# Kernel tuning notes

Hardware: AMD Instinct MI355X
Metric: run time of the kernel (lower is better)

## Reference

```python
import jax, jax.numpy as jnp
import numpy as np

DIM = 256
H = W = 56
WS = 7           # window size
SHIFT = 3        # shift size
NH = 8           # num heads
HD = DIM // NH   # head dim
N = WS * WS      # tokens per window
SCALE = HD ** -0.5
EPS = 1e-5


def _rel_pos_index():
    coords = np.stack(np.meshgrid(np.arange(WS), np.arange(WS), indexing='ij'))  # (2,WS,WS)
    cf = coords.reshape(2, -1)                                # (2, N)
    rel = cf[:, :, None] - cf[:, None, :]                     # (2, N, N)
    rel = rel.transpose(1, 2, 0).astype(np.int64)             # (N, N, 2)
    rel[:, :, 0] += WS - 1
    rel[:, :, 1] += WS - 1
    rel[:, :, 0] *= 2 * WS - 1
    return rel.sum(-1)                                        # (N, N)

REL_IDX = _rel_pos_index()


def _attn_mask():
    # standard Swin shift mask: (nW, N, N) with 0 / -100
    img = np.zeros((H, W))
    cnt = 0
    for hs in (slice(0, -WS), slice(-WS, -SHIFT), slice(-SHIFT, None)):
        for ws in (slice(0, -WS), slice(-WS, -SHIFT), slice(-SHIFT, None)):
            img[hs, ws] = cnt
            cnt += 1
    win = img.reshape(H // WS, WS, W // WS, WS).transpose(0, 2, 1, 3).reshape(-1, N)  # (nW, N)
    diff = win[:, None, :] - win[:, :, None]
    return np.where(diff != 0, -100.0, 0.0).astype(np.float32)

ATTN_MASK = jnp.asarray(_attn_mask())  # (nW, N, N)


def _ln(x, g, b):
    mu = jnp.mean(x, -1, keepdims=True)
    var = jnp.mean(jnp.square(x - mu), -1, keepdims=True)
    return (x - mu) * jax.lax.rsqrt(var + EPS) * g + b


def _win_part(x):
    # (B,H,W,C) -> (B*nW, N, C)
    B, _, _, C = x.shape
    x = x.reshape(B, H // WS, WS, W // WS, WS, C)
    return x.transpose(0, 1, 3, 2, 4, 5).reshape(-1, N, C)


def _win_rev(xw, B):
    # (B*nW, N, C) -> (B,H,W,C)
    C = xw.shape[-1]
    x = xw.reshape(B, H // WS, W // WS, WS, WS, C)
    return x.transpose(0, 1, 3, 2, 4, 5).reshape(B, H, W, C)


def setup_inputs() -> dict:
    key = jax.random.key(0)
    ks = jax.random.split(key, 6)
    return {
        'x': jax.random.normal(ks[0], (32, H * W, DIM), jnp.float32),
        'norm1_g': jnp.ones((DIM,), jnp.float32),
        'norm1_b': jnp.zeros((DIM,), jnp.float32),
        'qkv_w': jax.random.normal(ks[1], (3 * DIM, DIM), jnp.float32) * 0.02,
        'qkv_b': jnp.zeros((3 * DIM,), jnp.float32),
        'rel_table': jax.random.normal(ks[2], ((2 * WS - 1) ** 2, NH), jnp.float32) * 0.02,
        'proj_w': jax.random.normal(ks[3], (DIM, DIM), jnp.float32) * 0.02,
        'proj_b': jnp.zeros((DIM,), jnp.float32),
        'norm2_g': jnp.ones((DIM,), jnp.float32),
        'norm2_b': jnp.zeros((DIM,), jnp.float32),
        'fc1_w': jax.random.normal(ks[4], (4 * DIM, DIM), jnp.float32) * 0.02,
        'fc1_b': jnp.zeros((4 * DIM,), jnp.float32),
        'fc2_w': jax.random.normal(ks[5], (DIM, 4 * DIM), jnp.float32) * 0.02,
        'fc2_b': jnp.zeros((DIM,), jnp.float32),
    }


def reference(x, norm1_g, norm1_b, qkv_w, qkv_b, rel_table, proj_w, proj_b,
              norm2_g, norm2_b, fc1_w, fc1_b, fc2_w, fc2_b):
    B = x.shape[0]
    shortcut = x
    h = _ln(x, norm1_g, norm1_b).reshape(B, H, W, DIM)
    # cyclic shift
    h = jnp.roll(h, (-SHIFT, -SHIFT), axis=(1, 2))
    xw = _win_part(h)                                  # (B*nW, N, C)
    Bw = xw.shape[0]
    qkv = (xw @ qkv_w.T + qkv_b).reshape(Bw, N, 3, NH, HD).transpose(2, 0, 3, 1, 4)
    q, k, v = qkv[0] * SCALE, qkv[1], qkv[2]           # (Bw, NH, N, HD)
    attn = jnp.einsum('bhnd,bhmd->bhnm', q, k)         # (Bw, NH, N, N)
    bias = rel_table[REL_IDX.reshape(-1)].reshape(N, N, NH).transpose(2, 0, 1)
    attn = attn + bias[None]
    nW = ATTN_MASK.shape[0]
    attn = attn.reshape(B, nW, NH, N, N) + ATTN_MASK[None, :, None]
    attn = jax.nn.softmax(attn.reshape(Bw, NH, N, N), axis=-1)
    out = jnp.einsum('bhnm,bhmd->bhnd', attn, v).transpose(0, 2, 1, 3).reshape(Bw, N, DIM)
    out = out @ proj_w.T + proj_b
    h = _win_rev(out, B)
    h = jnp.roll(h, (SHIFT, SHIFT), axis=(1, 2)).reshape(B, H * W, DIM)
    x = shortcut + h
    y = _ln(x, norm2_g, norm2_b)
    y = jax.nn.gelu(y @ fc1_w.T + fc1_b, approximate=False)
    y = y @ fc2_w.T + fc2_b
    return x + y
```

## Files before the change

kernel.cpp:

```cpp
#include <hip/hip_runtime.h>


typedef float f4 __attribute__((ext_vector_type(4)));
typedef __bf16 b8 __attribute__((ext_vector_type(8)));

#define DEV static __device__ __forceinline__

DEV ushort f2bf(float f) {
  union { float f; unsigned u; } c; c.f = f;
  unsigned u = c.u;
  u += 0x7fffu + ((u >> 16) & 1u);
  return (ushort)(u >> 16);
}
DEV __bf16 bfb(ushort u) { union { ushort u; __bf16 b; } c; c.u = u; return c.b; }
DEV b8 zero_b8() {
  b8 z;
#pragma unroll
  for (int i = 0; i < 8; ++i) z[i] = (__bf16)0.f;
  return z;
}
DEV void load_lds16(const void* g, void* l) {
  __builtin_amdgcn_global_load_lds(
      (const __attribute__((address_space(1))) unsigned int*)g,
      (__attribute__((address_space(3))) unsigned int*)l, 16, 0, 0);
}
DEV int reg3(int t) { return t < 49 ? 0 : (t < 53 ? 1 : 2); }

__global__ __launch_bounds__(256) void cast_w(const float* a, ushort* oa, int na,
                                              const float* b, ushort* ob, int nb,
                                              const float* c, ushort* oc, int nc,
                                              const float* d, ushort* od, int nd) {
  int total = na + nb + nc + nd;
  for (int i = blockIdx.x * 256 + threadIdx.x; i < total; i += gridDim.x * 256) {
    int j = i;
    if (j < na) { oa[j] = f2bf(a[j]); continue; }
    j -= na;
    if (j < nb) { ob[j] = f2bf(b[j]); continue; }
    j -= nb;
    if (j < nc) { oc[j] = f2bf(c[j]); continue; }
    j -= nc;
    od[j] = f2bf(d[j]);
  }
}

__global__ __launch_bounds__(256) void build_bias(const float* __restrict__ rel_table,
                                                  float* __restrict__ comb) {
  const int idx = blockIdx.x * 256 + threadIdx.x;
  if (idx >= 4 * 8 * 64 * 64) return;
  const int j = idx & 63, i = (idx >> 6) & 63, h = (idx >> 12) & 7, ty = idx >> 15;
  float v;
  if (i < 49 && j < 49) {
    const int iy = i / 7, ix = i - iy * 7, jy = j / 7, jx = j - jy * 7;
    const int ridx = (iy - jy + 6) * 13 + (ix - jx + 6);
    v = rel_table[ridx * 8 + h];
    const int wh = (ty & 2) ? 7 : 0, ww = (ty & 1) ? 7 : 0;
    const int irg = reg3(wh * 7 + iy) * 3 + reg3(ww * 7 + ix);
    const int jrg = reg3(wh * 7 + jy) * 3 + reg3(ww * 7 + jx);
    if (irg != jrg) v -= 100.f;
  } else {
    v = -1e30f;
  }
  comb[idx] = v;
}

__global__ __launch_bounds__(256) void ln_shift(const float* __restrict__ x,
                                                const float* __restrict__ g,
                                                const float* __restrict__ bta,
                                                ushort* __restrict__ out, int shifted) {
  const int wid = threadIdx.x >> 6, lane = threadIdx.x & 63;
  const int t = blockIdx.x * 4 + wid;
  int src;
  if (shifted) {
    int win = t / 49, n = t - win * 49;
    int bb = win >> 6, wh = (win >> 3) & 7, ww = win & 7;
    int wy = n / 7, wx = n - wy * 7;
    int r = wh * 7 + wy + 3; if (r >= 56) r -= 56;
    int c = ww * 7 + wx + 3; if (c >= 56) c -= 56;
    src = bb * 3136 + r * 56 + c;
  } else {
    src = t;
  }
  const float4 v = *(const float4*)(x + (size_t)src * 256 + lane * 4);
  float s  = v.x + v.y + v.z + v.w;
  float s2 = v.x * v.x + v.y * v.y + v.z * v.z + v.w * v.w;
#pragma unroll
  for (int m = 32; m; m >>= 1) { s += __shfl_xor(s, m); s2 += __shfl_xor(s2, m); }
  const float mean = s * (1.f / 256.f);
  const float var  = s2 * (1.f / 256.f) - mean * mean;
  const float rs   = rsqrtf(var + 1e-5f);
  const float4 gv = *(const float4*)(g + lane * 4);
  const float4 bv = *(const float4*)(bta + lane * 4);
  ushort4 o;
  o.x = f2bf((v.x - mean) * rs * gv.x + bv.x);
  o.y = f2bf((v.y - mean) * rs * gv.y + bv.y);
  o.z = f2bf((v.z - mean) * rs * gv.z + bv.z);
  o.w = f2bf((v.w - mean) * rs * gv.w + bv.w);
  *(ushort4*)(out + (size_t)t * 256 + lane * 4) = o;
}

template <class Epi>
__global__ __launch_bounds__(256) void gemm_bt(const ushort* __restrict__ A,
                                               const ushort* __restrict__ B,
                                               int K, int NT, Epi epi) {
  __shared__ ushort lsA[2][128 * 32];
  __shared__ ushort lsB[2][128 * 32];
  const int tid = threadIdx.x;
  const int lane = tid & 63, wid = tid >> 6;
  const int quad = lane >> 4, l16 = lane & 15;
  const int wm = wid >> 1, wn = wid & 1;
  const int lin = blockIdx.x;
  const int xcd = lin & 7, j = lin >> 3;
  const int mt = xcd * 98 + j / NT;
  const int nt_ = j % NT;
  const long rowA0 = (long)mt * 128;
  const long colB0 = (long)nt_ * 128;
  f4 acc[4][4];
#pragma unroll
  for (int i = 0; i < 4; ++i)
#pragma unroll
    for (int jj = 0; jj < 4; ++jj) { acc[i][jj][0] = 0.f; acc[i][jj][1] = 0.f; acc[i][jj][2] = 0.f; acc[i][jj][3] = 0.f; }
  const int lrow = lane >> 2;
  const int lk = ((lane & 3) ^ ((lane >> 3) & 3)) * 8;
  const int rsw = (quad ^ ((l16 >> 1) & 3)) * 8;

  const int nsteps = K >> 5;
#pragma unroll
  for (int c = 0; c < 2; ++c) {
    const int seg = wid * 2 + c;
    const int row = seg * 16 + lrow;
    load_lds16(A + (rowA0 + row) * K + lk, &lsA[0][seg * 512]);
    load_lds16(B + (colB0 + row) * K + lk, &lsB[0][seg * 512]);
  }
  __syncthreads();

  for (int t = 0; t < nsteps; ++t) {
    const int cur = t & 1;
    if (t + 1 < nsteps) {
      const int k1 = (t + 1) << 5;
#pragma unroll
      for (int c = 0; c < 2; ++c) {
        const int seg = wid * 2 + c;
        const int row = seg * 16 + lrow;
        load_lds16(A + (rowA0 + row) * K + k1 + lk, &lsA[cur ^ 1][seg * 512]);
        load_lds16(B + (colB0 + row) * K + k1 + lk, &lsB[cur ^ 1][seg * 512]);
      }
    }
    b8 af[4], bfr[4];
#pragma unroll
    for (int ti = 0; ti < 4; ++ti)
      af[ti] = *(const b8*)&lsA[cur][(wm * 64 + ti * 16 + l16) * 32 + rsw];
#pragma unroll
    for (int tj = 0; tj < 4; ++tj)
      bfr[tj] = *(const b8*)&lsB[cur][(wn * 64 + tj * 16 + l16) * 32 + rsw];
#pragma unroll
    for (int ti = 0; ti < 4; ++ti)
#pragma unroll
      for (int tj = 0; tj < 4; ++tj)
        acc[ti][tj] = __builtin_amdgcn_mfma_f32_16x16x32_bf16(af[ti], bfr[tj], acc[ti][tj], 0, 0, 0);
    __syncthreads();
  }
#pragma unroll
  for (int ti = 0; ti < 4; ++ti)
#pragma unroll
    for (int tj = 0; tj < 4; ++tj)
#pragma unroll
      for (int r = 0; r < 4; ++r)
        epi((int)(rowA0 + wm * 64 + ti * 16 + quad * 4 + r),
            (int)(colB0 + wn * 64 + tj * 16 + l16), acc[ti][tj][r]);
}

struct QkvEpi {
  ushort* out; const float* bias;
  __device__ void operator()(int r, int c, float v) const {
    v += bias[c];
    if (c < 256) v *= 0.17677669529663687f;
    out[(size_t)r * 768 + c] = f2bf(v);
  }
};
struct GeluEpi {
  ushort* out; const float* bias;
  __device__ void operator()(int r, int c, float v) const {
    v += bias[c];
    v = 0.5f * v * (1.f + erff(v * 0.70710678118654752f));
    out[(size_t)r * 1024 + c] = f2bf(v);
  }
};
struct Fc2Epi {
  float* out; const float* bias;
  __device__ void operator()(int r, int c, float v) const {
    size_t i = (size_t)r * 256 + c;
    out[i] = out[i] + v + bias[c];
  }
};

__global__ __launch_bounds__(512) void attn_proj(const ushort* __restrict__ qkv,
                                                 const float* __restrict__ comb,
                                                 const ushort* __restrict__ projw,
                                                 const float* __restrict__ projb,
                                                 const float* __restrict__ x_in,
                                                 const float* __restrict__ n2g,
                                                 const float* __restrict__ n2b,
                                                 float* __restrict__ x_out,
                                                 ushort* __restrict__ xw2) {
  __shared__ ushort sbuf[32768];
  const int win = blockIdx.x;
  const int b = win >> 6, wh = (win >> 3) & 7, ww = win & 7;
  const int tid = threadIdx.x, lane = tid & 63, h = tid >> 6;
  const int quad = lane >> 4, l16 = lane & 15;
  const size_t wbase = (size_t)win * 49 * 768;

  b8 af[4], bfr[4];
#pragma unroll
  for (int ti = 0; ti < 4; ++ti) {
    const int tok = ti * 16 + l16;
    af[ti] = (tok < 49) ? *(const b8*)(qkv + wbase + (size_t)tok * 768 + h * 32 + quad * 8)
                        : zero_b8();
  }
#pragma unroll
  for (int tj = 0; tj < 4; ++tj) {
    const int key = tj * 16 + l16;
    bfr[tj] = (key < 49) ? *(const b8*)(qkv + wbase + (size_t)key * 768 + 256 + h * 32 + quad * 8)
                         : zero_b8();
  }
  f4 S[4][4];
#pragma unroll
  for (int ti = 0; ti < 4; ++ti)
#pragma unroll
    for (int tj = 0; tj < 4; ++tj) {
      S[ti][tj][0] = 0.f; S[ti][tj][1] = 0.f; S[ti][tj][2] = 0.f; S[ti][tj][3] = 0.f;
      S[ti][tj] = __builtin_amdgcn_mfma_f32_16x16x32_bf16(af[ti], bfr[tj], S[ti][tj], 0, 0, 0);
    }

  ushort* P = sbuf + h * 4096;
  const float* cmb = comb + ((((wh == 7) ? 2 : 0) + ((ww == 7) ? 1 : 0)) * 8 + h) * 4096;
#pragma unroll
  for (int ti = 0; ti < 4; ++ti) {
#pragma unroll
    for (int r = 0; r < 4; ++r) {
      const int i = ti * 16 + quad * 4 + r;
      const float* crow = cmb + i * 64 + l16;
      float sv[4];
#pragma unroll
      for (int tj = 0; tj < 4; ++tj) sv[tj] = S[ti][tj][r] + crow[tj * 16];
      float m = fmaxf(fmaxf(sv[0], sv[1]), fmaxf(sv[2], sv[3]));
#pragma unroll
      for (int d = 1; d < 16; d <<= 1) m = fmaxf(m, __shfl_xor(m, d));
      float sum = 0.f;
#pragma unroll
      for (int tj = 0; tj < 4; ++tj) { sv[tj] = __expf(sv[tj] - m); sum += sv[tj]; }
#pragma unroll
      for (int d = 1; d < 16; d <<= 1) sum += __shfl_xor(sum, d);
      const float inv = 1.f / sum;
      const int swz = i & 7, off = l16 & 7, cb = l16 >> 3;
#pragma unroll
      for (int tj = 0; tj < 4; ++tj) {
        const int cc = tj * 2 + cb;
        P[i * 64 + (((cc ^ swz) << 3) | off)] = f2bf(sv[tj] * inv);
      }
    }
  }

  f4 O[4][2];
#pragma unroll
  for (int ti = 0; ti < 4; ++ti)
#pragma unroll
    for (int tn = 0; tn < 2; ++tn) { O[ti][tn][0] = 0.f; O[ti][tn][1] = 0.f; O[ti][tn][2] = 0.f; O[ti][tn][3] = 0.f; }
#pragma unroll
  for (int kt = 0; kt < 2; ++kt) {
    b8 vb[2];
#pragma unroll
    for (int tn = 0; tn < 2; ++tn)
#pragma unroll
      for (int j = 0; j < 8; ++j) {
        const int key = kt * 32 + quad * 8 + j;
        vb[tn][j] = (key < 49)
            ? bfb(qkv[wbase + (size_t)key * 768 + 512 + h * 32 + tn * 16 + l16])
            : (__bf16)0.f;
      }
#pragma unroll
    for (int ti = 0; ti < 4; ++ti) {
      const int row = ti * 16 + l16;
      const b8 pa = *(const b8*)(P + row * 64 + (((kt * 4 + quad) ^ (row & 7)) << 3));
#pragma unroll
      for (int tn = 0; tn < 2; ++tn)
        O[ti][tn] = __builtin_amdgcn_mfma_f32_16x16x32_bf16(pa, vb[tn], O[ti][tn], 0, 0, 0);
    }
  }

  __syncthreads();
  ushort* ob = sbuf;
#pragma unroll
  for (int ti = 0; ti < 4; ++ti)
#pragma unroll
    for (int tn = 0; tn < 2; ++tn)
#pragma unroll
      for (int r = 0; r < 4; ++r) {
        const int tok = ti * 16 + quad * 4 + r;
        const int cc = h * 4 + tn * 2 + (l16 >> 3);
        ob[tok * 256 + (((cc ^ (tok & 7)) << 3) | (l16 & 7))] = f2bf(O[ti][tn][r]);
      }
  __syncthreads();

  f4 C[4][2];
#pragma unroll
  for (int ti = 0; ti < 4; ++ti)
#pragma unroll
    for (int tn = 0; tn < 2; ++tn) { C[ti][tn][0] = 0.f; C[ti][tn][1] = 0.f; C[ti][tn][2] = 0.f; C[ti][tn][3] = 0.f; }
  for (int k0 = 0; k0 < 256; k0 += 32) {
    b8 bw[2];
#pragma unroll
    for (int tn = 0; tn < 2; ++tn)
      bw[tn] = *(const b8*)(projw + (size_t)(h * 32 + tn * 16 + l16) * 256 + k0 + quad * 8);
#pragma unroll
    for (int ti = 0; ti < 4; ++ti) {
      const int row = ti * 16 + l16;
      const b8 pa = *(const b8*)(ob + row * 256 + ((((k0 >> 3) + quad) ^ (row & 7)) << 3));
#pragma unroll
      for (int tn = 0; tn < 2; ++tn)
        C[ti][tn] = __builtin_amdgcn_mfma_f32_16x16x32_bf16(pa, bw[tn], C[ti][tn], 0, 0, 0);
    }
  }

  __syncthreads();
  float* fbuf = (float*)sbuf;
#pragma unroll
  for (int ti = 0; ti < 4; ++ti)
#pragma unroll
    for (int r = 0; r < 4; ++r) {
      const int tok = ti * 16 + quad * 4 + r;
      const int swz = tok & 7;
#pragma unroll
      for (int tn = 0; tn < 2; ++tn) {
        const int c4 = h * 8 + tn * 4 + (l16 >> 2);
        fbuf[tok * 256 + (((c4 ^ swz) << 2) | (l16 & 3))] = C[ti][tn][r];
      }
    }
  __syncthreads();

  for (int t = h; t < 49; t += 8) {
    const int wy = t / 7, wx = t - wy * 7;
    int rr = wh * 7 + wy + 3; if (rr >= 56) rr -= 56;
    int cc = ww * 7 + wx + 3; if (cc >= 56) cc -= 56;
    const size_t base = ((size_t)b * 3136 + rr * 56 + cc) * 256;
    float4 v = *(float4*)&fbuf[t * 256 + ((lane ^ (t & 7)) << 2)];
    const float4 pb = *(const float4*)(projb + lane * 4);
    const float4 xr = *(const float4*)(x_in + base + lane * 4);
    v.x += pb.x + xr.x; v.y += pb.y + xr.y; v.z += pb.z + xr.z; v.w += pb.w + xr.w;
    *(float4*)(x_out + base + lane * 4) = v;
    float s  = v.x + v.y + v.z + v.w;
    float s2 = v.x * v.x + v.y * v.y + v.z * v.z + v.w * v.w;
#pragma unroll
    for (int m = 32; m; m >>= 1) { s += __shfl_xor(s, m); s2 += __shfl_xor(s2, m); }
    const float mean = s * (1.f / 256.f);
    const float var  = s2 * (1.f / 256.f) - mean * mean;
    const float rs   = rsqrtf(var + 1e-5f);
    const float4 gv = *(const float4*)(n2g + lane * 4);
    const float4 bv = *(const float4*)(n2b + lane * 4);
    ushort4 o;
    o.x = f2bf((v.x - mean) * rs * gv.x + bv.x);
    o.y = f2bf((v.y - mean) * rs * gv.y + bv.y);
    o.z = f2bf((v.z - mean) * rs * gv.z + bv.z);
    o.w = f2bf((v.w - mean) * rs * gv.w + bv.w);
    *(ushort4*)(xw2 + base + lane * 4) = o;
  }
}

extern "C" void kernel_launch(void* const* d_in, const int* in_sizes, int n_in,
                              void* d_out, int out_size, void* d_ws, size_t ws_size,
                              hipStream_t stream) {
  const float* x     = (const float*)d_in[0];
  const float* n1g   = (const float*)d_in[1];
  const float* n1b   = (const float*)d_in[2];
  const float* qkvw  = (const float*)d_in[3];
  const float* qkvb  = (const float*)d_in[4];
  const float* relt  = (const float*)d_in[5];
  const float* projw = (const float*)d_in[6];
  const float* projb = (const float*)d_in[7];
  const float* n2g   = (const float*)d_in[8];
  const float* n2b   = (const float*)d_in[9];
  const float* fc1w  = (const float*)d_in[10];
  const float* fc1b  = (const float*)d_in[11];
  const float* fc2w  = (const float*)d_in[12];
  const float* fc2b  = (const float*)d_in[13];
  float* out = (float*)d_out;
  char* ws = (char*)d_ws;

  ushort* xw     = (ushort*)ws;
  ushort* qkv    = (ushort*)(ws + 51380224);
  ushort* hidden = qkv;
  float*  comb   = (float*)(ws + 205520896);
  ushort* wqkv   = (ushort*)(ws + 51380224 + 205520896);
  ushort* wproj  = wqkv + 196608;
  ushort* wfc1   = wproj + 65536;
  ushort* wfc2   = wfc1 + 262144;

  cast_w<<<768, 256, 0, stream>>>(qkvw, wqkv, 196608, projw, wproj, 65536,
                                  fc1w, wfc1, 262144, fc2w, wfc2, 262144);
  build_bias<<<512, 256, 0, stream>>>(relt, comb);
  ln_shift<<<25088, 256, 0, stream>>>(x, n1g, n1b, xw, 1);
  gemm_bt<<<4704, 256, 0, stream>>>(xw, wqkv, 256, 6, QkvEpi{qkv, qkvb});
  attn_proj<<<2048, 512, 0, stream>>>(qkv, comb, wproj, projb, x, n2g, n2b, out, xw);
  gemm_bt<<<6272, 256, 0, stream>>>(xw, wfc1, 256, 8, GeluEpi{hidden, fc1b});
  gemm_bt<<<1568, 256, 0, stream>>>(hidden, wfc2, 1024, 2, Fc2Epi{out, fc2b});
}
```

Before: 678.7 us.

## Triple-buffer GEMM LDS tiles with explicit vmcnt waits for deeper prefetch

Changes the bf16 GEMM main loop from double to triple buffering in shared memory, issuing global-to-LDS loads two stages ahead. Full __syncthreads is replaced by raw s_barrier plus explicit s_waitcnt vmcnt counts, so a tile must have arrived before it is used while later tiles can still be in flight. It also precomputes the global row offsets. The aim is to hide global-load latency behind the MFMA work, at the cost of 50% more LDS per block (48KB), which may reduce occupancy, and of correctness depending on hand-tuned waitcnt values.

```diff
diff --git a/kernel.cpp b/kernel.cpp
--- a/kernel.cpp
+++ b/kernel.cpp
@@ -102,8 +102,8 @@
 __global__ __launch_bounds__(256) void gemm_bt(const ushort* __restrict__ A,
                                                const ushort* __restrict__ B,
                                                int K, int NT, Epi epi) {
-  __shared__ ushort lsA[2][128 * 32];
-  __shared__ ushort lsB[2][128 * 32];
+  __shared__ ushort lsA[3][128 * 32];
+  __shared__ ushort lsB[3][128 * 32];
   const int tid = threadIdx.x;
   const int lane = tid & 63, wid = tid >> 6;
   const int quad = lane >> 4, l16 = lane & 15;
@@ -122,29 +122,26 @@
   const int lrow = lane >> 2;
   const int lk = ((lane & 3) ^ ((lane >> 3) & 3)) * 8;
   const int rsw = (quad ^ ((l16 >> 1) & 3)) * 8;
+  const int seg0 = wid * 2, seg1 = wid * 2 + 1;
+  const long ga0 = (rowA0 + seg0 * 16 + lrow) * (long)K + lk;
+  const long ga1 = (rowA0 + seg1 * 16 + lrow) * (long)K + lk;
+  const long gb0 = (colB0 + seg0 * 16 + lrow) * (long)K + lk;
+  const long gb1 = (colB0 + seg1 * 16 + lrow) * (long)K + lk;
 
   const int nsteps = K >> 5;
 #pragma unroll
-  for (int c = 0; c < 2; ++c) {
-    const int seg = wid * 2 + c;
-    const int row = seg * 16 + lrow;
-    load_lds16(A + (rowA0 + row) * K + lk, &lsA[0][seg * 512]);
-    load_lds16(B + (colB0 + row) * K + lk, &lsB[0][seg * 512]);
-  }
-  __syncthreads();
-
+  for (int p = 0; p < 3; ++p) {
+    const int kk = p << 5;
+    load_lds16(A + ga0 + kk, &lsA[p][seg0 * 512]);
+    load_lds16(A + ga1 + kk, &lsA[p][seg1 * 512]);
+    load_lds16(B + gb0 + kk, &lsB[p][seg0 * 512]);
+    load_lds16(B + gb1 + kk, &lsB[p][seg1 * 512]);
+  }
+  asm volatile("s_waitcnt vmcnt(8)" ::: "memory");
+  __builtin_amdgcn_s_barrier();
+
+  int cur = 0;
   for (int t = 0; t < nsteps; ++t) {
-    const int cur = t & 1;
-    if (t + 1 < nsteps) {
-      const int k1 = (t + 1) << 5;
-#pragma unroll
-      for (int c = 0; c < 2; ++c) {
-        const int seg = wid * 2 + c;
-        const int row = seg * 16 + lrow;
-        load_lds16(A + (rowA0 + row) * K + k1 + lk, &lsA[cur ^ 1][seg * 512]);
-        load_lds16(B + (colB0 + row) * K + k1 + lk, &lsB[cur ^ 1][seg * 512]);
-      }
-    }
     b8 af[4], bfr[4];
 #pragma unroll
     for (int ti = 0; ti < 4; ++ti)
@@ -157,7 +154,21 @@
 #pragma unroll
       for (int tj = 0; tj < 4; ++tj)
         acc[ti][tj] = __builtin_amdgcn_mfma_f32_16x16x32_bf16(af[ti], bfr[tj], acc[ti][tj], 0, 0, 0);
-    __syncthreads();
+    __builtin_amdgcn_s_barrier();
+    if (t + 3 < nsteps) {
+      const int kk = (t + 3) << 5;
+      load_lds16(A + ga0 + kk, &lsA[cur][seg0 * 512]);
+      load_lds16(A + ga1 + kk, &lsA[cur][seg1 * 512]);
+      load_lds16(B + gb0 + kk, &lsB[cur][seg0 * 512]);
+      load_lds16(B + gb1 + kk, &lsB[cur][seg1 * 512]);
+      asm volatile("s_waitcnt vmcnt(8)" ::: "memory");
+    } else if (t + 2 < nsteps) {
+      asm volatile("s_waitcnt vmcnt(4)" ::: "memory");
+    } else if (t + 1 < nsteps) {
+      asm volatile("s_waitcnt vmcnt(0)" ::: "memory");
+    }
+    __builtin_amdgcn_s_barrier();
+    cur = cur == 2 ? 0 : cur + 1;
   }
 #pragma unroll
   for (int ti = 0; ti < 4; ++ti)
```

Result: slower. 693.3 us (+2.1%).

## Fuse fc1+GELU and fc2 into one MLP kernel keeping hidden in LDS

Applied to the files above, without the earlier changes.

Replaces the two MLP GEMM launches with one fused kernel. Each block takes 64 rows, computes the 1024-wide hidden activation in chunks of 128 with GELU, stages each chunk in LDS, and accumulates the fc2 output in registers. This removes the round trip of the 100k x 1024 bf16 hidden tensor through global memory. In exchange, the weights are read directly from global memory rather than staged through LDS, and each block does a long serial loop with many syncthreads and a large register-held accumulator, which can lower occupancy.

```diff
diff --git a/kernel.cpp b/kernel.cpp
--- a/kernel.cpp
+++ b/kernel.cpp
@@ -177,21 +177,97 @@
     out[(size_t)r * 768 + c] = f2bf(v);
   }
 };
-struct GeluEpi {
-  ushort* out; const float* bias;
-  __device__ void operator()(int r, int c, float v) const {
-    v += bias[c];
-    v = 0.5f * v * (1.f + erff(v * 0.70710678118654752f));
-    out[(size_t)r * 1024 + c] = f2bf(v);
-  }
-};
-struct Fc2Epi {
-  float* out; const float* bias;
-  __device__ void operator()(int r, int c, float v) const {
-    size_t i = (size_t)r * 256 + c;
-    out[i] = out[i] + v + bias[c];
-  }
-};
+
+__global__ __launch_bounds__(256) void mlp_fused(const ushort* __restrict__ A,
+                                                 const ushort* __restrict__ w1,
+                                                 const float* __restrict__ b1,
+                                                 const ushort* __restrict__ w2,
+                                                 const float* __restrict__ b2,
+                                                 float* __restrict__ out) {
+  __shared__ ushort lsA[8][64 * 32];
+  __shared__ ushort lsH[64 * 128];
+  const int tid = threadIdx.x, lane = tid & 63, wid = tid >> 6;
+  const int quad = lane >> 4, l16 = lane & 15;
+  const long r0 = (long)blockIdx.x * 64;
+  const int lrow = lane >> 2;
+  const int lk = ((lane & 3) ^ ((lane >> 3) & 3)) * 8;
+  const int rsw = (quad ^ ((l16 >> 1) & 3)) * 8;
+
+#pragma unroll
+  for (int kc = 0; kc < 8; ++kc)
+    load_lds16(A + (r0 + wid * 16 + lrow) * 256 + kc * 32 + lk, &lsA[kc][wid * 512]);
+
+  f4 acc2[4][4];
+#pragma unroll
+  for (int ti = 0; ti < 4; ++ti)
+#pragma unroll
+    for (int tn = 0; tn < 4; ++tn) { acc2[ti][tn][0] = 0.f; acc2[ti][tn][1] = 0.f; acc2[ti][tn][2] = 0.f; acc2[ti][tn][3] = 0.f; }
+  __syncthreads();
+
+  for (int nc = 0; nc < 8; ++nc) {
+    f4 acc1[4][2];
+#pragma unroll
+    for (int ti = 0; ti < 4; ++ti)
+#pragma unroll
+      for (int tc = 0; tc < 2; ++tc) { acc1[ti][tc][0] = 0.f; acc1[ti][tc][1] = 0.f; acc1[ti][tc][2] = 0.f; acc1[ti][tc][3] = 0.f; }
+#pragma unroll
+    for (int kc = 0; kc < 8; ++kc) {
+      b8 bw[2];
+#pragma unroll
+      for (int tc = 0; tc < 2; ++tc)
+        bw[tc] = *(const b8*)(w1 + (size_t)(nc * 128 + wid * 32 + tc * 16 + l16) * 256 + kc * 32 + quad * 8);
+#pragma unroll
+      for (int ti = 0; ti < 4; ++ti) {
+        const b8 af = *(const b8*)&lsA[kc][(ti * 16 + l16) * 32 + rsw];
+#pragma unroll
+        for (int tc = 0; tc < 2; ++tc)
+          acc1[ti][tc] = __builtin_amdgcn_mfma_f32_16x16x32_bf16(af, bw[tc], acc1[ti][tc], 0, 0, 0);
+      }
+    }
+    __syncthreads();
+    float bv0 = b1[nc * 128 + wid * 32 + l16];
+    float bv1 = b1[nc * 128 + wid * 32 + 16 + l16];
+#pragma unroll
+    for (int ti = 0; ti < 4; ++ti)
+#pragma unroll
+      for (int tc = 0; tc < 2; ++tc)
+#pragma unroll
+        for (int rr = 0; rr < 4; ++rr) {
+          const int row = ti * 16 + quad * 4 + rr;
+          const int c = wid * 32 + tc * 16 + l16;
+          float v = acc1[ti][tc][rr] + (tc ? bv1 : bv0);
+          v = 0.5f * v * (1.f + erff(v * 0.70710678118654752f));
+          lsH[row * 128 + ((((c >> 3) ^ ((row & 7) << 1)) << 3) | (c & 7))] = f2bf(v);
+        }
+    __syncthreads();
+#pragma unroll
+    for (int ks = 0; ks < 4; ++ks) {
+      b8 bw2[4];
+#pragma unroll
+      for (int tn = 0; tn < 4; ++tn)
+        bw2[tn] = *(const b8*)(w2 + (size_t)(wid * 64 + tn * 16 + l16) * 1024 + nc * 128 + ks * 32 + quad * 8);
+#pragma unroll
+      for (int ti = 0; ti < 4; ++ti) {
+        const int row = ti * 16 + l16;
+        const b8 pa = *(const b8*)&lsH[row * 128 + (((ks * 4 + quad) ^ ((row & 7) << 1)) << 3)];
+#pragma unroll
+        for (int tn = 0; tn < 4; ++tn)
+          acc2[ti][tn] = __builtin_amdgcn_mfma_f32_16x16x32_bf16(pa, bw2[tn], acc2[ti][tn], 0, 0, 0);
+      }
+    }
+  }
+#pragma unroll
+  for (int tn = 0; tn < 4; ++tn) {
+    const float bb = b2[wid * 64 + tn * 16 + l16];
+#pragma unroll
+    for (int ti = 0; ti < 4; ++ti)
+#pragma unroll
+      for (int rr = 0; rr < 4; ++rr) {
+        const size_t i = (size_t)(r0 + ti * 16 + quad * 4 + rr) * 256 + wid * 64 + tn * 16 + l16;
+        out[i] += acc2[ti][tn][rr] + bb;
+      }
+  }
+}
 
 __global__ __launch_bounds__(512) void attn_proj(const ushort* __restrict__ qkv,
                                                  const float* __restrict__ comb,
@@ -387,7 +463,6 @@
 
   ushort* xw     = (ushort*)ws;
   ushort* qkv    = (ushort*)(ws + 51380224);
-  ushort* hidden = qkv;
   float*  comb   = (float*)(ws + 205520896);
   ushort* wqkv   = (ushort*)(ws + 51380224 + 205520896);
   ushort* wproj  = wqkv + 196608;
@@ -400,6 +475,5 @@
   ln_shift<<<25088, 256, 0, stream>>>(x, n1g, n1b, xw, 1);
   gemm_bt<<<4704, 256, 0, stream>>>(xw, wqkv, 256, 6, QkvEpi{qkv, qkvb});
   attn_proj<<<2048, 512, 0, stream>>>(qkv, comb, wproj, projb, x, n2g, n2b, out, xw);
-  gemm_bt<<<6272, 256, 0, stream>>>(xw, wfc1, 256, 8, GeluEpi{hidden, fc1b});
-  gemm_bt<<<1568, 256, 0, stream>>>(hidden, wfc2, 1024, 2, Fc2Epi{out, fc2b});
-}
+  mlp_fused<<<1568, 256, 0, stream>>>(xw, wfc1, fc1b, wfc2, fc2b, out);
+}
```

Result: slower. 713.0 us (+5.0%).
